# Kernel tuning notes

Measured on AMD Instinct MI355X. Metric: run time of the kernel, lower is better.

## Reference

```python
import jax, jax.numpy as jnp
import numpy as np

W = 8            # fine window (sqrt of feat_0's WW)
WP2 = W + 2      # feat_1 search window side (10)
SLICE = 8
TEMP = 10.0


def setup_inputs() -> dict:
    key = jax.random.key(0)
    ks = jax.random.split(key, 6)
    M = 8192
    C = 64
    return {
        'feat_0': jax.random.normal(ks[0], (M, W * W, C), dtype=jnp.float32),
        'feat_1': jax.random.normal(ks[1], (M, WP2 * WP2, C), dtype=jnp.float32),
        'mkpts0_c': jax.random.uniform(ks[2], (M, 2), dtype=jnp.float32) * 800.0,
        'mkpts1_c': jax.random.uniform(ks[3], (M, 2), dtype=jnp.float32) * 800.0,
        'mconf': jax.random.uniform(ks[4], (M,), dtype=jnp.float32),
        'b_ids': jnp.zeros((M,), dtype=jnp.int64),
        'hw0_i': 832,
        'hw0_f': 416,
        'bs': 1,
    }


def reference(feat_0, feat_1, mkpts0_c, mkpts1_c, mconf, b_ids, hw0_i, hw0_f, bs):
    M, WW, C = feat_0.shape                      # WW = W*W = 64
    scale = float(hw0_i) / float(hw0_f)          # image -> fine-feature stride

    feat_f0, feat_ff0 = feat_0[..., :-SLICE], feat_0[..., -SLICE:]
    feat_f1, feat_ff1 = feat_1[..., :-SLICE], feat_1[..., -SLICE:]

    # note: BOTH sides divided by sqrt(C) in the source -> overall 1/C
    conf_f = jnp.einsum('mlc,mrc->mlr', feat_f0, feat_f1) * (1.0 / C)          # [M,64,100]
    conf_ff = jnp.einsum('mlc,mrc->mlr', feat_ff0, feat_ff1) / np.sqrt(SLICE)  # [M,64,100]

    # dual softmax, then crop the 10x10 search window to the inner 8x8
    sm = jax.nn.softmax(conf_f, axis=1) * jax.nn.softmax(conf_f, axis=2)
    sm = sm.reshape(M, WW, WP2, WP2)[..., 1:-1, 1:-1].reshape(M, WW, WW)       # [M,64,64]

    # ---- get_fine_ds_match (torch.no_grad in source) ----
    flat = jax.lax.stop_gradient(sm.reshape(M, WW * WW))
    idx = jnp.argmax(flat, axis=-1)                # [M]
    idx_l, idx_r = idx // WW, idx % WW             # each in [0,64)
    gy, gx = jnp.meshgrid(jnp.arange(W), jnp.arange(W), indexing='ij')
    grid = (jnp.stack([gx, gy], -1).reshape(WW, 2).astype(feat_0.dtype)
            - (W // 2) + 0.5)                      # (x,y) pixel offsets, centered
    delta_l = grid[idx_l]                          # [M,2]
    delta_r = grid[idx_r]
    mkpts0_f = jax.lax.stop_gradient(mkpts0_c) + delta_l * scale
    mkpts1_mid = jax.lax.stop_gradient(mkpts1_c) + delta_r * scale

    # ---- 3x3 window gather in the (W+2)x(W+2) map (faithful index arithmetic) ----
    iids, jids = idx_r // W, idx_r % W             # [0,8)
    d = jnp.arange(3) - 1                          # {-1,0,1}
    wi = iids[:, None, None] + d[None, :, None]    # [M,3,3] rows, may be -1
    wj = jids[:, None, None] + d[None, None, :]    # [M,3,3] cols
    wi = jnp.where(wi < 0, wi + WP2, wi)           # torch negative-index wrap
    wj = jnp.where(wj < 0, wj + WP2, wj)
    cff = conf_ff.reshape(M, WW, WP2, WP2)
    win = cff[jnp.arange(M)[:, None, None], idx_l[:, None, None], wi, wj]  # [M,3,3]

    probs = jax.nn.softmax(win.reshape(M, 9) / TEMP, axis=-1)              # [M,9]
    heat = probs.reshape(M, 3, 3)
    pos = jnp.linspace(-1.0, 1.0, 3).astype(feat_0.dtype)
    coord_x = jnp.sum(heat * pos[None, None, :], axis=(1, 2))              # over width
    coord_y = jnp.sum(heat * pos[None, :, None], axis=(1, 2))              # over height
    coords = jnp.stack([coord_x, coord_y], -1)     # [M,2] soft-argmax, (x,y)

    scale1 = scale                                 # bs == 1 branch
    mkpts1_f = mkpts1_mid + coords * (3 // 2) * scale1
    return (mkpts0_f, mkpts1_f, probs, sm)
```

## Files before the change

### kernel.cpp

```cpp
#include <hip/hip_runtime.h>
#include <math.h>
#include <limits.h>


constexpr int TPB = 256;

__global__ __launch_bounds__(TPB, 3) void fine_matching_kernel(
    const float* __restrict__ feat0,
    const float* __restrict__ feat1,
    const float* __restrict__ mk0,
    const float* __restrict__ mk1,
    const int* __restrict__ hw0_i,
    const int* __restrict__ hw0_f,
    float* __restrict__ out, int M)
{
    constexpr int F0S = 68;
    constexpr int F1S = 68;

    __shared__ float s_f0[64 * F0S];
    __shared__ float s_f1[100 * F1S];
    __shared__ float s_ff0[64 * 8];
    __shared__ float s_rsum[64];
    __shared__ float s_cpart[4][112];
    __shared__ float s_csum[112];
    __shared__ float s_wval[4];
    __shared__ int   s_widx[4];
    __shared__ float s_win[9];

    const int m = blockIdx.x;
    const int t = threadIdx.x;
    const int w = t >> 6;
    const float scale = (float)hw0_i[0] / (float)hw0_f[0];

    const float* g0 = feat0 + (size_t)m * 4096;
    const float* g1 = feat1 + (size_t)m * 6400;

    for (int i = t; i < 1024; i += TPB) {
        float4 v = ((const float4*)g0)[i];
        int fl = i << 2; int l = fl >> 6; int c = fl & 63;
        *(float4*)&s_f0[l * F0S + c] = v;
    }
    for (int i = t; i < 1600; i += TPB) {
        float4 v = ((const float4*)g1)[i];
        int fl = i << 2; int l = fl >> 6; int c = fl & 63;
        *(float4*)&s_f1[l * F1S + c] = v;
    }
    __syncthreads();

    for (int i = t; i < 512; i += TPB) {
        int l = i >> 3, c = i & 7;
        s_ff0[i] = s_f0[l * F0S + 56 + c];
    }

    const int tr = t & 15;
    const int l0 = (t >> 4) * 4;
    int  boff[7];
    bool rmask[7];
    #pragma unroll
    for (int jj = 0; jj < 7; jj++) {
        int r = tr + 16 * jj;
        rmask[jj] = (r < 100);
        boff[jj] = (rmask[jj] ? r : 99) * F1S;
    }

    float acc[4][7];
    #pragma unroll
    for (int j = 0; j < 4; j++)
        #pragma unroll
        for (int jj = 0; jj < 7; jj++) acc[j][jj] = 0.0f;

    for (int k = 0; k < 56; k += 4) {
        float4 a[4], b[7];
        #pragma unroll
        for (int j = 0; j < 4; j++) a[j] = *(const float4*)&s_f0[(l0 + j) * F0S + k];
        #pragma unroll
        for (int jj = 0; jj < 7; jj++) b[jj] = *(const float4*)&s_f1[boff[jj] + k];
        #pragma unroll
        for (int j = 0; j < 4; j++)
            #pragma unroll
            for (int jj = 0; jj < 7; jj++)
                acc[j][jj] += a[j].x * b[jj].x + a[j].y * b[jj].y
                            + a[j].z * b[jj].z + a[j].w * b[jj].w;
    }

    #pragma unroll
    for (int j = 0; j < 4; j++)
        #pragma unroll
        for (int jj = 0; jj < 7; jj++) {
            float c = acc[j][jj] * (1.0f / 64.0f);
            acc[j][jj] = rmask[jj] ? __expf(c) : 0.0f;
        }

    float prow[4];
    #pragma unroll
    for (int j = 0; j < 4; j++) {
        float s = 0.0f;
        #pragma unroll
        for (int jj = 0; jj < 7; jj++) s += acc[j][jj];
        prow[j] = s;
    }
    #pragma unroll
    for (int d = 1; d < 16; d <<= 1)
        #pragma unroll
        for (int j = 0; j < 4; j++) prow[j] += __shfl_xor(prow[j], d);
    if (tr == 0) {
        #pragma unroll
        for (int j = 0; j < 4; j++) s_rsum[l0 + j] = prow[j];
    }

    float pcol[7];
    #pragma unroll
    for (int jj = 0; jj < 7; jj++)
        pcol[jj] = acc[0][jj] + acc[1][jj] + acc[2][jj] + acc[3][jj];
    #pragma unroll
    for (int jj = 0; jj < 7; jj++) {
        pcol[jj] += __shfl_xor(pcol[jj], 16);
        pcol[jj] += __shfl_xor(pcol[jj], 32);
    }
    if ((t & 63) < 16) {
        #pragma unroll
        for (int jj = 0; jj < 7; jj++) s_cpart[w][tr + 16 * jj] = pcol[jj];
    }
    __syncthreads();
    if (t < 112)
        s_csum[t] = s_cpart[0][t] + s_cpart[1][t] + s_cpart[2][t] + s_cpart[3][t];
    __syncthreads();

    float invr[4], invc[7];
    #pragma unroll
    for (int j = 0; j < 4; j++) invr[j] = 1.0f / s_rsum[l0 + j];
    #pragma unroll
    for (int jj = 0; jj < 7; jj++)
        invc[jj] = rmask[jj] ? (1.0f / s_csum[tr + 16 * jj]) : 0.0f;

    float* s_sm = s_f0;
    float bestv = -INFINITY; int besti = INT_MAX;
    #pragma unroll
    for (int j = 0; j < 4; j++) {
        int l = l0 + j;
        #pragma unroll
        for (int jj = 0; jj < 7; jj++) {
            if (rmask[jj]) {
                int r = tr + 16 * jj;
                int ri = r / 10, rj = r % 10;
                if (ri >= 1 && ri <= 8 && rj >= 1 && rj <= 8) {
                    float p = acc[j][jj];
                    float v = p * p * invr[j] * invc[jj];
                    int flat = l * 64 + (ri - 1) * 8 + (rj - 1);
                    s_sm[flat] = v;
                    if (v > bestv) { bestv = v; besti = flat; }
                }
            }
        }
    }
    #pragma unroll
    for (int d = 1; d < 64; d <<= 1) {
        float ov = __shfl_xor(bestv, d);
        int   oi = __shfl_xor(besti, d);
        if (ov > bestv || (ov == bestv && oi < besti)) { bestv = ov; besti = oi; }
    }
    if ((t & 63) == 0) { s_wval[w] = bestv; s_widx[w] = besti; }
    __syncthreads();

    float bv = s_wval[0]; int best = s_widx[0];
    #pragma unroll
    for (int i = 1; i < 4; i++) {
        float v2 = s_wval[i]; int i2 = s_widx[i];
        if (v2 > bv || (v2 == bv && i2 < best)) { bv = v2; best = i2; }
    }
    const int idx_l = best >> 6;
    const int idx_r = best & 63;
    const int iids  = idx_r >> 3, jids = idx_r & 7;

    float* o_sm = out + (size_t)13 * M + (size_t)m * 4096;
    for (int i = t; i < 1024; i += TPB)
        ((float4*)o_sm)[i] = ((const float4*)s_sm)[i];

    if (t < 9) {
        int da = t / 3 - 1, db = t % 3 - 1;
        int wi = iids + da; if (wi < 0) wi += 10;
        int wj = jids + db; if (wj < 0) wj += 10;
        int rp = wi * 10 + wj;
        float dot = 0.0f;
        #pragma unroll
        for (int c = 0; c < 8; c++)
            dot += s_ff0[idx_l * 8 + c] * s_f1[rp * F1S + 56 + c];
        s_win[t] = dot * 0.35355339059327373f;
    }
    __syncthreads();

    if (t == 0) {
        float ww[9], mx = -INFINITY;
        #pragma unroll
        for (int i = 0; i < 9; i++) { ww[i] = s_win[i] * 0.1f; mx = fmaxf(mx, ww[i]); }
        float sum = 0.0f;
        #pragma unroll
        for (int i = 0; i < 9; i++) { ww[i] = __expf(ww[i] - mx); sum += ww[i]; }
        float inv = 1.0f / sum;
        float* o_probs = out + (size_t)4 * M + (size_t)m * 9;
        float cx = 0.0f, cy = 0.0f;
        #pragma unroll
        for (int i = 0; i < 9; i++) {
            float p = ww[i] * inv;
            o_probs[i] = p;
            cx += p * (float)(i % 3 - 1);
            cy += p * (float)(i / 3 - 1);
        }
        float dlx = (float)(idx_l & 7) - 3.5f;
        float dly = (float)(idx_l >> 3) - 3.5f;
        out[2 * m]     = mk0[2 * m]     + dlx * scale;
        out[2 * m + 1] = mk0[2 * m + 1] + dly * scale;
        float drx = (float)jids - 3.5f;
        float dry = (float)iids - 3.5f;
        float* o1 = out + (size_t)2 * M;
        o1[2 * m]     = mk1[2 * m]     + (drx + cx) * scale;
        o1[2 * m + 1] = mk1[2 * m + 1] + (dry + cy) * scale;
    }
}

extern "C" void kernel_launch(void* const* d_in, const int* in_sizes, int n_in,
                              void* d_out, int out_size, void* d_ws, size_t ws_size,
                              hipStream_t stream) {
    const float* feat0 = (const float*)d_in[0];
    const float* feat1 = (const float*)d_in[1];
    const float* mk0   = (const float*)d_in[2];
    const float* mk1   = (const float*)d_in[3];
    const int*   hw0_i = (const int*)d_in[6];
    const int*   hw0_f = (const int*)d_in[7];
    const int M = in_sizes[0] / 4096;

    fine_matching_kernel<<<M, TPB, 0, stream>>>(
        feat0, feat1, mk0, mk1, hw0_i, hw0_f, (float*)d_out, M);
}
```

Before: 485.2 us.

## Compute dual-softmax similarity with split-fp16 MFMA instead of FP32 FMA

```diff
diff --git a/kernel.cpp b/kernel.cpp
--- a/kernel.cpp
+++ b/kernel.cpp
@@ -4,6 +4,29 @@
 
 
 constexpr int TPB = 256;
+
+typedef _Float16 half8_t __attribute__((ext_vector_type(8)));
+typedef _Float16 half4_t __attribute__((ext_vector_type(4)));
+typedef float    float4_t __attribute__((ext_vector_type(4)));
+
+struct __align__(16) SMem {
+    union {
+        struct {
+            unsigned short f1h[100 * 56];
+            unsigned short f1l[100 * 56];
+        };
+        float sm[64 * 64];
+    };
+    unsigned short f0h[64 * 56];
+    unsigned short f0l[64 * 56];
+    float ff0[64 * 8];
+    float ff1[100 * 8];
+    float cpart[4][112];
+    float csum[112];
+    float wval[4];
+    int   widx[4];
+    float win[9];
+};
 
 __global__ __launch_bounds__(TPB, 3) void fine_matching_kernel(
     const float* __restrict__ feat0,
@@ -14,138 +37,147 @@
     const int* __restrict__ hw0_f,
     float* __restrict__ out, int M)
 {
-    constexpr int F0S = 68;
-    constexpr int F1S = 68;
-
-    __shared__ float s_f0[64 * F0S];
-    __shared__ float s_f1[100 * F1S];
-    __shared__ float s_ff0[64 * 8];
-    __shared__ float s_rsum[64];
-    __shared__ float s_cpart[4][112];
-    __shared__ float s_csum[112];
-    __shared__ float s_wval[4];
-    __shared__ int   s_widx[4];
-    __shared__ float s_win[9];
+    __shared__ SMem S;
 
     const int m = blockIdx.x;
     const int t = threadIdx.x;
+    const int lane = t & 63;
     const int w = t >> 6;
+    const int col = lane & 15;
+    const int q = lane >> 4;
     const float scale = (float)hw0_i[0] / (float)hw0_f[0];
 
     const float* g0 = feat0 + (size_t)m * 4096;
     const float* g1 = feat1 + (size_t)m * 6400;
+    _Float16* f0h = (_Float16*)S.f0h;
+    _Float16* f0l = (_Float16*)S.f0l;
+    _Float16* f1h = (_Float16*)S.f1h;
+    _Float16* f1l = (_Float16*)S.f1l;
 
     for (int i = t; i < 1024; i += TPB) {
-        float4 v = ((const float4*)g0)[i];
-        int fl = i << 2; int l = fl >> 6; int c = fl & 63;
-        *(float4*)&s_f0[l * F0S + c] = v;
+        float4_t v = ((const float4_t*)g0)[i];
+        int fl = i << 2, l = fl >> 6, c = fl & 63;
+        if (c < 56) {
+            half4_t hi, lo;
+            #pragma unroll
+            for (int j = 0; j < 4; j++) {
+                float x = v[j];
+                _Float16 h = (_Float16)x;
+                hi[j] = h;
+                lo[j] = (_Float16)(x - (float)h);
+            }
+            *(half4_t*)(f0h + l * 56 + c) = hi;
+            *(half4_t*)(f0l + l * 56 + c) = lo;
+        } else {
+            *(float4_t*)&S.ff0[l * 8 + (c - 56)] = v;
+        }
     }
     for (int i = t; i < 1600; i += TPB) {
-        float4 v = ((const float4*)g1)[i];
-        int fl = i << 2; int l = fl >> 6; int c = fl & 63;
-        *(float4*)&s_f1[l * F1S + c] = v;
-    }
-    __syncthreads();
-
-    for (int i = t; i < 512; i += TPB) {
-        int l = i >> 3, c = i & 7;
-        s_ff0[i] = s_f0[l * F0S + 56 + c];
-    }
-
-    const int tr = t & 15;
-    const int l0 = (t >> 4) * 4;
-    int  boff[7];
-    bool rmask[7];
-    #pragma unroll
-    for (int jj = 0; jj < 7; jj++) {
-        int r = tr + 16 * jj;
-        rmask[jj] = (r < 100);
-        boff[jj] = (rmask[jj] ? r : 99) * F1S;
-    }
-
-    float acc[4][7];
-    #pragma unroll
-    for (int j = 0; j < 4; j++)
-        #pragma unroll
-        for (int jj = 0; jj < 7; jj++) acc[j][jj] = 0.0f;
-
-    for (int k = 0; k < 56; k += 4) {
-        float4 a[4], b[7];
-        #pragma unroll
-        for (int j = 0; j < 4; j++) a[j] = *(const float4*)&s_f0[(l0 + j) * F0S + k];
-        #pragma unroll
-        for (int jj = 0; jj < 7; jj++) b[jj] = *(const float4*)&s_f1[boff[jj] + k];
-        #pragma unroll
-        for (int j = 0; j < 4; j++)
+        float4_t v = ((const float4_t*)g1)[i];
+        int fl = i << 2, l = fl >> 6, c = fl & 63;
+        if (c < 56) {
+            half4_t hi, lo;
             #pragma unroll
-            for (int jj = 0; jj < 7; jj++)
-                acc[j][jj] += a[j].x * b[jj].x + a[j].y * b[jj].y
-                            + a[j].z * b[jj].z + a[j].w * b[jj].w;
-    }
-
-    #pragma unroll
-    for (int j = 0; j < 4; j++)
-        #pragma unroll
-        for (int jj = 0; jj < 7; jj++) {
-            float c = acc[j][jj] * (1.0f / 64.0f);
-            acc[j][jj] = rmask[jj] ? __expf(c) : 0.0f;
-        }
-
-    float prow[4];
+            for (int j = 0; j < 4; j++) {
+                float x = v[j];
+                _Float16 h = (_Float16)x;
+                hi[j] = h;
+                lo[j] = (_Float16)(x - (float)h);
+            }
+            *(half4_t*)(f1h + l * 56 + c) = hi;
+            *(half4_t*)(f1l + l * 56 + c) = lo;
+        } else {
+            *(float4_t*)&S.ff1[l * 8 + (c - 56)] = v;
+        }
+    }
+    __syncthreads();
+
+    float4_t acc[7];
+    #pragma unroll
+    for (int rt = 0; rt < 7; rt++)
+        #pragma unroll
+        for (int j = 0; j < 4; j++) acc[rt][j] = 0.0f;
+
+    half8_t hz;
+    #pragma unroll
+    for (int j = 0; j < 8; j++) hz[j] = (_Float16)0.0f;
+
+    const int arow = (16 * w + col) * 56;
+    #pragma unroll
+    for (int ks = 0; ks < 2; ks++) {
+        int koff = ks ? (32 + q * 8) : (q * 8);
+        const bool kz = (ks == 1) && (q == 3);
+        if (kz) koff = 0;
+        half8_t ah = *(const half8_t*)(f0h + arow + koff);
+        half8_t al = *(const half8_t*)(f0l + arow + koff);
+        if (kz) { ah = hz; al = hz; }
+        #pragma unroll
+        for (int rt = 0; rt < 7; rt++) {
+            int brow = rt * 16 + col;
+            if (brow > 99) brow = 99;
+            const int bo = brow * 56 + koff;
+            half8_t bh = *(const half8_t*)(f1h + bo);
+            half8_t bl = *(const half8_t*)(f1l + bo);
+            acc[rt] = __builtin_amdgcn_mfma_f32_16x16x32_f16(ah, bh, acc[rt], 0, 0, 0);
+            acc[rt] = __builtin_amdgcn_mfma_f32_16x16x32_f16(al, bh, acc[rt], 0, 0, 0);
+            acc[rt] = __builtin_amdgcn_mfma_f32_16x16x32_f16(ah, bl, acc[rt], 0, 0, 0);
+        }
+    }
+
+    float p[7][4];
+    #pragma unroll
+    for (int rt = 0; rt < 7; rt++) {
+        const bool rvalid = (rt < 6) || (col < 4);
+        #pragma unroll
+        for (int j = 0; j < 4; j++) {
+            float c = acc[rt][j] * (1.0f / 64.0f);
+            p[rt][j] = rvalid ? __expf(c) : 0.0f;
+        }
+    }
+
+    float invr[4];
     #pragma unroll
     for (int j = 0; j < 4; j++) {
         float s = 0.0f;
         #pragma unroll
-        for (int jj = 0; jj < 7; jj++) s += acc[j][jj];
-        prow[j] = s;
-    }
-    #pragma unroll
-    for (int d = 1; d < 16; d <<= 1)
-        #pragma unroll
-        for (int j = 0; j < 4; j++) prow[j] += __shfl_xor(prow[j], d);
-    if (tr == 0) {
-        #pragma unroll
-        for (int j = 0; j < 4; j++) s_rsum[l0 + j] = prow[j];
-    }
-
-    float pcol[7];
-    #pragma unroll
-    for (int jj = 0; jj < 7; jj++)
-        pcol[jj] = acc[0][jj] + acc[1][jj] + acc[2][jj] + acc[3][jj];
-    #pragma unroll
-    for (int jj = 0; jj < 7; jj++) {
-        pcol[jj] += __shfl_xor(pcol[jj], 16);
-        pcol[jj] += __shfl_xor(pcol[jj], 32);
-    }
-    if ((t & 63) < 16) {
-        #pragma unroll
-        for (int jj = 0; jj < 7; jj++) s_cpart[w][tr + 16 * jj] = pcol[jj];
+        for (int rt = 0; rt < 7; rt++) s += p[rt][j];
+        s += __shfl_xor(s, 1); s += __shfl_xor(s, 2);
+        s += __shfl_xor(s, 4); s += __shfl_xor(s, 8);
+        invr[j] = 1.0f / s;
+    }
+
+    #pragma unroll
+    for (int rt = 0; rt < 7; rt++) {
+        float s = p[rt][0] + p[rt][1] + p[rt][2] + p[rt][3];
+        s += __shfl_xor(s, 16);
+        s += __shfl_xor(s, 32);
+        if (lane < 16) S.cpart[w][rt * 16 + col] = s;
     }
     __syncthreads();
     if (t < 112)
-        s_csum[t] = s_cpart[0][t] + s_cpart[1][t] + s_cpart[2][t] + s_cpart[3][t];
-    __syncthreads();
-
-    float invr[4], invc[7];
-    #pragma unroll
-    for (int j = 0; j < 4; j++) invr[j] = 1.0f / s_rsum[l0 + j];
-    #pragma unroll
-    for (int jj = 0; jj < 7; jj++)
-        invc[jj] = rmask[jj] ? (1.0f / s_csum[tr + 16 * jj]) : 0.0f;
-
-    float* s_sm = s_f0;
+        S.csum[t] = S.cpart[0][t] + S.cpart[1][t] + S.cpart[2][t] + S.cpart[3][t];
+    __syncthreads();
+
+    float invc[7];
+    #pragma unroll
+    for (int rt = 0; rt < 7; rt++) {
+        const bool rvalid = (rt < 6) || (col < 4);
+        invc[rt] = rvalid ? 1.0f / S.csum[rt * 16 + col] : 0.0f;
+    }
+
+    float* s_sm = S.sm;
     float bestv = -INFINITY; int besti = INT_MAX;
     #pragma unroll
     for (int j = 0; j < 4; j++) {
-        int l = l0 + j;
-        #pragma unroll
-        for (int jj = 0; jj < 7; jj++) {
-            if (rmask[jj]) {
-                int r = tr + 16 * jj;
-                int ri = r / 10, rj = r % 10;
+        const int l = 16 * w + 4 * q + j;
+        #pragma unroll
+        for (int rt = 0; rt < 7; rt++) {
+            const int r = rt * 16 + col;
+            if (r < 100) {
+                const int ri = r / 10, rj = r - ri * 10;
                 if (ri >= 1 && ri <= 8 && rj >= 1 && rj <= 8) {
-                    float p = acc[j][jj];
-                    float v = p * p * invr[j] * invc[jj];
+                    float pv = p[rt][j];
+                    float v = pv * pv * invr[j] * invc[rt];
                     int flat = l * 64 + (ri - 1) * 8 + (rj - 1);
                     s_sm[flat] = v;
                     if (v > bestv) { bestv = v; besti = flat; }
@@ -159,13 +191,13 @@
         int   oi = __shfl_xor(besti, d);
         if (ov > bestv || (ov == bestv && oi < besti)) { bestv = ov; besti = oi; }
     }
-    if ((t & 63) == 0) { s_wval[w] = bestv; s_widx[w] = besti; }
-    __syncthreads();
-
-    float bv = s_wval[0]; int best = s_widx[0];
+    if (lane == 0) { S.wval[w] = bestv; S.widx[w] = besti; }
+    __syncthreads();
+
+    float bv = S.wval[0]; int best = S.widx[0];
     #pragma unroll
     for (int i = 1; i < 4; i++) {
-        float v2 = s_wval[i]; int i2 = s_widx[i];
+        float v2 = S.wval[i]; int i2 = S.widx[i];
         if (v2 > bv || (v2 == bv && i2 < best)) { bv = v2; best = i2; }
     }
     const int idx_l = best >> 6;
@@ -174,7 +206,7 @@
 
     float* o_sm = out + (size_t)13 * M + (size_t)m * 4096;
     for (int i = t; i < 1024; i += TPB)
-        ((float4*)o_sm)[i] = ((const float4*)s_sm)[i];
+        ((float4_t*)o_sm)[i] = ((const float4_t*)s_sm)[i];
 
     if (t < 9) {
         int da = t / 3 - 1, db = t % 3 - 1;
@@ -184,15 +216,15 @@
         float dot = 0.0f;
         #pragma unroll
         for (int c = 0; c < 8; c++)
-            dot += s_ff0[idx_l * 8 + c] * s_f1[rp * F1S + 56 + c];
-        s_win[t] = dot * 0.35355339059327373f;
+            dot += S.ff0[idx_l * 8 + c] * S.ff1[rp * 8 + c];
+        S.win[t] = dot * 0.35355339059327373f;
     }
     __syncthreads();
 
     if (t == 0) {
         float ww[9], mx = -INFINITY;
         #pragma unroll
-        for (int i = 0; i < 9; i++) { ww[i] = s_win[i] * 0.1f; mx = fmaxf(mx, ww[i]); }
+        for (int i = 0; i < 9; i++) { ww[i] = S.win[i] * 0.1f; mx = fmaxf(mx, ww[i]); }
         float sum = 0.0f;
         #pragma unroll
         for (int i = 0; i < 9; i++) { ww[i] = __expf(ww[i] - mx); sum += ww[i]; }
@@ -201,10 +233,10 @@
         float cx = 0.0f, cy = 0.0f;
         #pragma unroll
         for (int i = 0; i < 9; i++) {
-            float p = ww[i] * inv;
-            o_probs[i] = p;
-            cx += p * (float)(i % 3 - 1);
-            cy += p * (float)(i / 3 - 1);
+            float pb = ww[i] * inv;
+            o_probs[i] = pb;
+            cx += pb * (float)(i % 3 - 1);
+            cy += pb * (float)(i / 3 - 1);
         }
         float dlx = (float)(idx_l & 7) - 3.5f;
         float dly = (float)(idx_l >> 3) - 3.5f;
```

Result: faster. 458.0 us (-5.6%).
